# Optimization experiments

Measured on AMD Instinct MI355X. Metric: run time of the kernel, lower is better.

The kernel has to match this reference:

```python
import jax, jax.numpy as jnp
import numpy as np

C, K, DIL = 128, 3, 1
PAD = DIL
KK = K * K
EPS = 1e-5


def setup_inputs() -> dict:
    key = jax.random.key(0)
    k0, k1, k2 = jax.random.split(key, 3)
    B, H, W = 8, 128, 128
    x = jax.random.normal(k0, (B, C, H, W), jnp.float32)
    # small offset-conv weights so predicted offsets are realistic (sub-pixel scale)
    w_off = jax.random.normal(k1, (2 * KK, C, K, K), jnp.float32) * 0.01
    b_off = jnp.zeros((2 * KK,), jnp.float32)
    w_dw = jax.random.normal(k2, (C, 1, K, K), jnp.float32) * (1.0 / 3.0)
    gamma = jnp.ones((C,), jnp.float32)
    beta = jnp.zeros((C,), jnp.float32)
    return {"x": x, "w_off": w_off, "b_off": b_off, "w_dw": w_dw,
            "gamma": gamma, "beta": beta}


def _deform_depthwise(x, offset, w_dw):
    """torchvision-style deform_conv2d, groups=C (depthwise), stride=1."""
    B, C_, H, W = x.shape
    off = offset.reshape(B, KK, 2, H, W)  # (y,x) pairs per kernel tap
    hs = jnp.arange(H, dtype=x.dtype)[None, None, :, None]
    ws = jnp.arange(W, dtype=x.dtype)[None, None, None, :]
    ki = jnp.arange(K, dtype=x.dtype)
    ky = jnp.repeat(ki, K)  # [KK] row index of tap
    kx = jnp.tile(ki, K)    # [KK] col index of tap
    # sampling positions: base grid + dilated tap offset - pad + learned offset
    py = hs + (DIL * ky - PAD)[None, :, None, None] + off[:, :, 0]  # [B,KK,H,W]
    px = ws + (DIL * kx - PAD)[None, :, None, None] + off[:, :, 1]
    y0 = jnp.floor(py)
    x0 = jnp.floor(px)
    ty = py - y0
    tx = px - x0
    y0i = y0.astype(jnp.int32)
    x0i = x0.astype(jnp.int32)

    def gather(xb, yi, xi):
        # zero outside the image (torchvision zero-pad semantics)
        valid = (yi >= 0) & (yi < H) & (xi >= 0) & (xi < W)
        yc = jnp.clip(yi, 0, H - 1)
        xc = jnp.clip(xi, 0, W - 1)
        v = xb[:, yc, xc]  # [C,KK,H,W]
        return v * valid[None].astype(xb.dtype)

    def sample_one(xb, y0b, x0b, tyb, txb):
        v00 = gather(xb, y0b, x0b)
        v01 = gather(xb, y0b, x0b + 1)
        v10 = gather(xb, y0b + 1, x0b)
        v11 = gather(xb, y0b + 1, x0b + 1)
        w00 = (1 - tyb) * (1 - txb)
        w01 = (1 - tyb) * txb
        w10 = tyb * (1 - txb)
        w11 = tyb * txb
        return (v00 * w00[None] + v01 * w01[None]
                + v10 * w10[None] + v11 * w11[None])  # [C,KK,H,W]

    val = jax.vmap(sample_one)(x, y0i, x0i, ty, tx)  # [B,C,KK,H,W]
    # depthwise contraction over the KK taps
    return jnp.einsum('bckhw,ck->bchw', val, w_dw.reshape(C, KK))


def reference(x, w_off, b_off, w_dw, gamma, beta):
    identity = x
    offset = jax.lax.conv_general_dilated(
        x, w_off, window_strides=(1, 1), padding=[(PAD, PAD), (PAD, PAD)],
        dimension_numbers=('NCHW', 'OIHW', 'NCHW'))
    offset = offset + b_off[None, :, None, None]
    out = _deform_depthwise(x, offset, w_dw)
    # BatchNorm2d in training mode (batch statistics), then SiLU
    mean = jnp.mean(out, axis=(0, 2, 3), keepdims=True)
    var = jnp.mean((out - mean) ** 2, axis=(0, 2, 3), keepdims=True)
    out = (out - mean) * jax.lax.rsqrt(var + EPS)
    out = out * gamma[None, :, None, None] + beta[None, :, None, None]
    out = out * jax.nn.sigmoid(out)  # SiLU
    return out + identity
```

## Files before the change

kernel.cpp:

```cpp
#include <hip/hip_runtime.h>
#include <hip/hip_fp16.h>
#include <math.h>

#define Cc 128
#define Hh 128
#define Ww 128
#define Bb 8
#define HW 16384
#define NPIX 131072
#define NOFF 18

typedef unsigned int u32;
typedef __attribute__((ext_vector_type(8)))  short bf16x8;
typedef __attribute__((ext_vector_type(16))) float f32x16;

static __device__ __forceinline__ u32 f2bf(float f){
  u32 u = __float_as_uint(f);
  return (u + 0x7fffu + ((u >> 16) & 1u)) >> 16;
}

__global__ __launch_bounds__(256) void k_repack(const float* __restrict__ w_off, const float* __restrict__ w_dw,
                                                u32* __restrict__ wBf, float* __restrict__ wdt){
  int i = blockIdx.x*256 + threadIdx.x;
  if (i < 72*64*4){
    int step = i >> 8;
    int r    = i & 255;
    int lane = r >> 2;
    int q    = r & 3;
    int tap  = step / 8, chunk = step % 8;
    int o    = lane & 31, half = lane >> 5;
    int c0   = chunk*16 + half*8 + 2*q;
    float v0 = (o < NOFF) ? w_off[(size_t)(o*Cc + c0    )*9 + tap] : 0.f;
    float v1 = (o < NOFF) ? w_off[(size_t)(o*Cc + c0 + 1)*9 + tap] : 0.f;
    wBf[i] = f2bf(v0) | (f2bf(v1) << 16);
  }
  int j = i - 72*64*4;
  if (j >= 0 && j < 9*Cc){
    int c = j % Cc; int k = j / Cc;
    wdt[j] = w_dw[c*9 + k];
  }
}

__global__ __launch_bounds__(256) void k_tx(const float* __restrict__ x, u32* __restrict__ xt16){
  __shared__ float t[128][65];
  int tid = threadIdx.x;
  int b   = blockIdx.x >> 8;
  int hw0 = (blockIdx.x & 255) << 6;
  int lane = tid & 63, wg = tid >> 6;
  const float* xb = x + (size_t)b*Cc*HW;
  #pragma unroll
  for (int k=0;k<32;k++){
    int c = wg + k*4;
    t[c][lane] = xb[(size_t)c*HW + hw0 + lane];
  }
  __syncthreads();
  u32* ob = xt16 + ((size_t)b*HW + hw0)*64;
  int cpair = tid & 63, grp = tid >> 6;
  #pragma unroll
  for (int k=0;k<16;k++){
    int hwl = grp + k*4;
    float lo = t[cpair*2][hwl];
    float hi = t[cpair*2+1][hwl];
    ob[(size_t)hwl*64 + cpair] = f2bf(lo) | (f2bf(hi) << 16);
  }
}

__global__ __launch_bounds__(256) void k_offset_mfma(const u32* __restrict__ xt, const u32* __restrict__ wBf,
                                                     const float* __restrict__ b_off, u32* __restrict__ recs){
  __shared__ float piv[128][21];
  int tid = threadIdx.x, lane = tid & 63, wid = tid >> 6;
  int b = blockIdx.x >> 7, h = blockIdx.x & 127;
  int row = lane & 31, half = lane >> 5;
  int w0 = wid*32;
  int w = w0 + row;

  const u32* xb = xt + (size_t)b*HW*64;

  int taddr[9]; bool tval[9];
  #pragma unroll
  for (int t=0;t<9;t++){
    int ky = t/3 - 1, kx = t%3 - 1;
    int hh = h + ky, wt = w + kx;
    bool v = (hh>=0)&&(hh<Hh)&&(wt>=0)&&(wt<Ww);
    int hwd = hh*Ww + wt;
    hwd = min(max(hwd,0),HW-1);
    taddr[t] = hwd*64 + half*4;
    tval[t] = v;
  }

  f32x16 acc;
  #pragma unroll
  for (int i=0;i<16;i++) acc[i] = 0.f;

  const uint4* wb = (const uint4*)wBf;
  #pragma unroll 1
  for (int t=0;t<9;t++){
    const uint4* ap = (const uint4*)(xb + taddr[t]);
    bool v = tval[t];
    #pragma unroll
    for (int ch=0;ch<8;ch++){
      uint4 a = ap[ch*2];
      if (!v){ a.x=0u; a.y=0u; a.z=0u; a.w=0u; }
      uint4 bf = wb[(t*8+ch)*64 + lane];
      acc = __builtin_amdgcn_mfma_f32_32x32x16_bf16(*(bf16x8*)&a, *(bf16x8*)&bf, acc, 0, 0, 0);
    }
  }

  int o = lane & 31;
  #pragma unroll
  for (int r=0;r<16;r++){
    int pxl = w0 + ((r&3) + 8*(r>>2) + 4*half);
    if (o < NOFF) piv[pxl][o] = acc[r];
  }
  __syncthreads();

  if (tid < 128){
    int wpx = tid;
    float v[NOFF];
    #pragma unroll
    for (int oo=0;oo<NOFF;oo++) v[oo] = piv[wpx][oo] + b_off[oo];

    u32 rec[36];
    #pragma unroll
    for (int kk=0;kk<9;kk++){
      float py = (float)(h + kk/3 - 1) + v[2*kk];
      float qx = (float)(wpx + kk%3 - 1) + v[2*kk+1];
      float fy = floorf(py), fx = floorf(qx);
      float ty = py - fy, tx = qx - fx;
      int y0 = (int)fy, x0 = (int)fx;
      int y1 = y0+1, x1 = x0+1;
      bool vy0 = (y0>=0)&&(y0<Hh), vy1=(y1>=0)&&(y1<Hh);
      bool vx0 = (x0>=0)&&(x0<Ww), vx1=(x1>=0)&&(x1<Ww);
      u32 yc0 = (u32)(min(max(y0,0),Hh-1)*Ww), yc1 = (u32)(min(max(y1,0),Hh-1)*Ww);
      u32 xc0 = (u32)min(max(x0,0),Ww-1),      xc1 = (u32)min(max(x1,0),Ww-1);
      rec[2*kk]   = (yc0+xc0) | ((yc0+xc1)<<16);
      rec[2*kk+1] = (yc1+xc0) | ((yc1+xc1)<<16);
      float c00 = (vy0&&vx0) ? (1.f-ty)*(1.f-tx) : 0.f;
      float c01 = (vy0&&vx1) ? (1.f-ty)*tx       : 0.f;
      float c10 = (vy1&&vx0) ? ty*(1.f-tx)       : 0.f;
      float c11 = (vy1&&vx1) ? ty*tx             : 0.f;
      __half2 hA = __floats2half2_rn(c00, c01);
      __half2 hB = __floats2half2_rn(c10, c11);
      rec[18+2*kk] = *(u32*)&hA;
      rec[19+2*kk] = *(u32*)&hB;
    }
    int pxg = blockIdx.x*128 + wpx;
    uint4* dst = (uint4*)(recs + (size_t)pxg*36);
    #pragma unroll
    for (int q=0;q<9;q++) dst[q] = *(uint4*)(rec + q*4);
  }
}

__global__ __launch_bounds__(256) void k_deform_rec(const u32* __restrict__ xt, const u32* __restrict__ recs,
                                                    const float* __restrict__ wdt, float* __restrict__ out){
  __shared__ float pivot[16][132];
  int tid = threadIdx.x, lane = tid & 63, wid = tid >> 6;
  int pxb = blockIdx.x * 16;
  int bu = pxb >> 14, hw0 = pxb & 16383;
  int l2 = lane*2;

  float2 wk[9];
  #pragma unroll
  for (int k=0;k<9;k++) wk[k] = *(const float2*)(wdt + k*Cc + l2);

  const u32* xbu = xt + (size_t)bu*HW*64;

  #pragma unroll
  for (int i=0;i<4;i++){
    int pu = __builtin_amdgcn_readfirstlane(pxb + wid*4 + i);
    const u32* rec = recs + (size_t)pu*36;

    u32 q[9][4];
    #pragma unroll
    for (int kk=0;kk<9;kk++){
      u32 dA = rec[2*kk], dB = rec[2*kk+1];
      q[kk][0] = xbu[(size_t)(dA & 0xFFFFu)*64 + lane];
      q[kk][1] = xbu[(size_t)(dA >> 16)   *64 + lane];
      q[kk][2] = xbu[(size_t)(dB & 0xFFFFu)*64 + lane];
      q[kk][3] = xbu[(size_t)(dB >> 16)   *64 + lane];
    }

    float acc0 = 0.f, acc1 = 0.f;
    #pragma unroll
    for (int kk=0;kk<9;kk++){
      u32 uA = rec[18+2*kk], uB = rec[19+2*kk];
      __half2 hA = *(__half2*)&uA, hB = *(__half2*)&uB;
      float c00 = __low2float(hA), c01 = __high2float(hA);
      float c10 = __low2float(hB), c11 = __high2float(hB);
      float v0l = __uint_as_float(q[kk][0] << 16), v0h = __uint_as_float(q[kk][0] & 0xffff0000u);
      float v1l = __uint_as_float(q[kk][1] << 16), v1h = __uint_as_float(q[kk][1] & 0xffff0000u);
      float v2l = __uint_as_float(q[kk][2] << 16), v2h = __uint_as_float(q[kk][2] & 0xffff0000u);
      float v3l = __uint_as_float(q[kk][3] << 16), v3h = __uint_as_float(q[kk][3] & 0xffff0000u);
      float s0 = c00*v0l; s0 = fmaf(c01, v1l, s0); s0 = fmaf(c10, v2l, s0); s0 = fmaf(c11, v3l, s0);
      float s1 = c00*v0h; s1 = fmaf(c01, v1h, s1); s1 = fmaf(c10, v2h, s1); s1 = fmaf(c11, v3h, s1);
      acc0 = fmaf(wk[kk].x, s0, acc0);
      acc1 = fmaf(wk[kk].y, s1, acc1);
    }
    pivot[wid*4+i][l2]   = acc0;
    pivot[wid*4+i][l2+1] = acc1;
  }
  __syncthreads();
  #pragma unroll
  for (int it=0; it<2; it++){
    int c = (tid>>2) + it*64, qd = tid & 3;
    float4 r = make_float4(pivot[qd*4+0][c], pivot[qd*4+1][c], pivot[qd*4+2][c], pivot[qd*4+3][c]);
    *(float4*)(out + ((size_t)bu*Cc + c)*HW + hw0 + qd*4) = r;
  }
}

__global__ __launch_bounds__(256) void k_stats1(const float* __restrict__ dw, float* __restrict__ ps){
  int c = blockIdx.x >> 3, b = blockIdx.x & 7;
  const float4* p = (const float4*)(dw + ((size_t)b*Cc + c)*HW);
  float s = 0.f, s2 = 0.f;
  for (int i=threadIdx.x; i<HW/4; i+=256){
    float4 v = p[i];
    s += v.x + v.y + v.z + v.w;
    s2 = fmaf(v.x, v.x, s2); s2 = fmaf(v.y, v.y, s2);
    s2 = fmaf(v.z, v.z, s2); s2 = fmaf(v.w, v.w, s2);
  }
  #pragma unroll
  for (int d=32; d>0; d>>=1){ s += __shfl_down(s, d, 64); s2 += __shfl_down(s2, d, 64); }
  __shared__ float ls[4], ls2[4];
  int lane = threadIdx.x & 63, wid = threadIdx.x >> 6;
  if (lane==0){ ls[wid]=s; ls2[wid]=s2; }
  __syncthreads();
  if (threadIdx.x==0){
    float S=0.f, S2=0.f;
    #pragma unroll
    for (int i=0;i<4;i++){ S+=ls[i]; S2+=ls2[i]; }
    ps[c*8+b] = S;
    ps[1024 + c*8+b] = S2;
  }
}

__global__ __launch_bounds__(128) void k_stats2(const float* __restrict__ ps, float* __restrict__ mr){
  int c = threadIdx.x;
  float S=0.f, S2=0.f;
  #pragma unroll
  for (int b=0;b<8;b++){ S += ps[c*8+b]; S2 += ps[1024 + c*8+b]; }
  const float invN = 1.f/(float)(Bb*HW);
  float m = S*invN;
  float var = S2*invN - m*m;
  mr[c]      = m;
  mr[Cc + c] = rsqrtf(var + 1e-5f);
}

__global__ __launch_bounds__(256) void k_apply(float* __restrict__ out, const float* __restrict__ x,
                                               const float* __restrict__ mr, const float* __restrict__ gamma,
                                               const float* __restrict__ beta){
  int i = blockIdx.x*256 + threadIdx.x;
  int c = (i >> 12) & 127;
  float4 v  = ((const float4*)out)[i];
  float4 xi = ((const float4*)x)[i];
  float m = mr[c], r = mr[Cc+c], g = gamma[c], be = beta[c];
  float* vp = (float*)&v; const float* xp = (const float*)&xi;
  float4 o; float* op = (float*)&o;
  #pragma unroll
  for (int j=0;j<4;j++){
    float t = (vp[j]-m)*r*g + be;
    t = t / (1.f + expf(-t));
    op[j] = t + xp[j];
  }
  ((float4*)out)[i] = o;
}

extern "C" void kernel_launch(void* const* d_in, const int* in_sizes, int n_in,
                              void* d_out, int out_size, void* d_ws, size_t ws_size,
                              hipStream_t stream) {
  const float* x     = (const float*)d_in[0];
  const float* w_off = (const float*)d_in[1];
  const float* b_off = (const float*)d_in[2];
  const float* w_dw  = (const float*)d_in[3];
  const float* gamma = (const float*)d_in[4];
  const float* beta  = (const float*)d_in[5];
  float* out = (float*)d_out;

  u32*   wBf = (u32*)d_ws;
  float* wdt = (float*)d_ws + 23040;
  float* mr  = (float*)d_ws + 24576;
  float* ps  = mr + 256;
  u32* recs  = (u32*)d_ws + 32768;
  u32* xt16  = recs + (size_t)NPIX*36;

  hipLaunchKernelGGL(k_repack, dim3((72*64*4 + 9*Cc + 255)/256), dim3(256), 0, stream, w_off, w_dw, wBf, wdt);
  hipLaunchKernelGGL(k_tx,     dim3(2048), dim3(256), 0, stream, x, xt16);
  hipLaunchKernelGGL(k_offset_mfma, dim3(1024), dim3(256), 0, stream, xt16, wBf, b_off, recs);
  hipLaunchKernelGGL(k_deform_rec,  dim3(NPIX/16), dim3(256), 0, stream, xt16, recs, wdt, out);
  hipLaunchKernelGGL(k_stats1, dim3(Cc*Bb), dim3(256), 0, stream, out, ps);
  hipLaunchKernelGGL(k_stats2, dim3(1),     dim3(128), 0, stream, ps, mr);
  hipLaunchKernelGGL(k_apply,  dim3(NPIX*Cc/4/256), dim3(256), 0, stream, out, x, mr, gamma, beta);
}
```

Baseline: 178.3 us.

## Fuse BN statistics into deform kernel and store intermediate as bf16

The deformable depthwise kernel now computes per-block partial sums and sums of squares for each channel. This replaces the separate stats pass, which re-read the whole fp32 intermediate. When the workspace is large enough, the intermediate is also written as bf16 to a workspace buffer, halving its write and read traffic, and the apply kernel decodes it. The cost is a two-stage reduction over 8192 block partials, plus reduced precision of the pre-BN activations, which could affect accuracy.

```diff
diff --git a/kernel.cpp b/kernel.cpp
--- a/kernel.cpp
+++ b/kernel.cpp
@@ -151,8 +151,10 @@
   }
 }
 
+template<bool BF16OUT>
 __global__ __launch_bounds__(256) void k_deform_rec(const u32* __restrict__ xt, const u32* __restrict__ recs,
-                                                    const float* __restrict__ wdt, float* __restrict__ out){
+                                                    const float* __restrict__ wdt, float* __restrict__ out,
+                                                    u32* __restrict__ dwb, float* __restrict__ bps){
   __shared__ float pivot[16][132];
   int tid = threadIdx.x, lane = tid & 63, wid = tid >> 6;
   int pxb = blockIdx.x * 16;
@@ -204,50 +206,53 @@
   for (int it=0; it<2; it++){
     int c = (tid>>2) + it*64, qd = tid & 3;
     float4 r = make_float4(pivot[qd*4+0][c], pivot[qd*4+1][c], pivot[qd*4+2][c], pivot[qd*4+3][c]);
-    *(float4*)(out + ((size_t)bu*Cc + c)*HW + hw0 + qd*4) = r;
-  }
-}
-
-__global__ __launch_bounds__(256) void k_stats1(const float* __restrict__ dw, float* __restrict__ ps){
-  int c = blockIdx.x >> 3, b = blockIdx.x & 7;
-  const float4* p = (const float4*)(dw + ((size_t)b*Cc + c)*HW);
-  float s = 0.f, s2 = 0.f;
-  for (int i=threadIdx.x; i<HW/4; i+=256){
-    float4 v = p[i];
-    s += v.x + v.y + v.z + v.w;
-    s2 = fmaf(v.x, v.x, s2); s2 = fmaf(v.y, v.y, s2);
-    s2 = fmaf(v.z, v.z, s2); s2 = fmaf(v.w, v.w, s2);
-  }
-  #pragma unroll
-  for (int d=32; d>0; d>>=1){ s += __shfl_down(s, d, 64); s2 += __shfl_down(s2, d, 64); }
-  __shared__ float ls[4], ls2[4];
-  int lane = threadIdx.x & 63, wid = threadIdx.x >> 6;
-  if (lane==0){ ls[wid]=s; ls2[wid]=s2; }
+    float s  = (r.x + r.y) + (r.z + r.w);
+    float s2 = fmaf(r.x,r.x, fmaf(r.y,r.y, fmaf(r.z,r.z, r.w*r.w)));
+    s  += __shfl_down(s, 2, 4);  s  += __shfl_down(s, 1, 4);
+    s2 += __shfl_down(s2, 2, 4); s2 += __shfl_down(s2, 1, 4);
+    if (qd == 0){
+      bps[(size_t)blockIdx.x*256 + c]       = s;
+      bps[(size_t)blockIdx.x*256 + 128 + c] = s2;
+    }
+    if (BF16OUT){
+      u32 p0 = f2bf(r.x) | (f2bf(r.y) << 16);
+      u32 p1 = f2bf(r.z) | (f2bf(r.w) << 16);
+      uint2 pp; pp.x = p0; pp.y = p1;
+      *(uint2*)&dwb[(((size_t)bu*Cc + c)*HW + hw0)/2 + qd*2] = pp;
+    } else {
+      *(float4*)(out + ((size_t)bu*Cc + c)*HW + hw0 + qd*4) = r;
+    }
+  }
+}
+
+__global__ __launch_bounds__(256) void k_statsr1(const float* __restrict__ bps, float* __restrict__ part2){
+  int tid = threadIdx.x;
+  size_t base = (size_t)blockIdx.x * 64;
+  float a = 0.f;
+  for (int r=0;r<64;r++) a += bps[(base + r)*256 + tid];
+  part2[blockIdx.x*256 + tid] = a;
+}
+
+__global__ __launch_bounds__(256) void k_statsr2(const float* __restrict__ part2, float* __restrict__ mr){
+  __shared__ float t[256];
+  int tid = threadIdx.x;
+  float a = 0.f;
+  for (int r=0;r<128;r++) a += part2[r*256 + tid];
+  t[tid] = a;
   __syncthreads();
-  if (threadIdx.x==0){
-    float S=0.f, S2=0.f;
-    #pragma unroll
-    for (int i=0;i<4;i++){ S+=ls[i]; S2+=ls2[i]; }
-    ps[c*8+b] = S;
-    ps[1024 + c*8+b] = S2;
-  }
-}
-
-__global__ __launch_bounds__(128) void k_stats2(const float* __restrict__ ps, float* __restrict__ mr){
-  int c = threadIdx.x;
-  float S=0.f, S2=0.f;
-  #pragma unroll
-  for (int b=0;b<8;b++){ S += ps[c*8+b]; S2 += ps[1024 + c*8+b]; }
-  const float invN = 1.f/(float)(Bb*HW);
-  float m = S*invN;
-  float var = S2*invN - m*m;
-  mr[c]      = m;
-  mr[Cc + c] = rsqrtf(var + 1e-5f);
-}
-
-__global__ __launch_bounds__(256) void k_apply(float* __restrict__ out, const float* __restrict__ x,
-                                               const float* __restrict__ mr, const float* __restrict__ gamma,
-                                               const float* __restrict__ beta){
+  if (tid < 128){
+    float S = t[tid], S2 = t[128 + tid];
+    const float invN = 1.f/(float)(Bb*HW);
+    float m = S*invN;
+    float var = S2*invN - m*m;
+    mr[tid]       = m;
+    mr[Cc + tid]  = rsqrtf(var + 1e-5f);
+  }
+}
+
+__global__ __launch_bounds__(256) void k_apply_f32(float* __restrict__ out, const float* __restrict__ x,
+                                                   const float* __restrict__ mr, const float* __restrict__ gamma,
+                                                   const float* __restrict__ beta){
   int i = blockIdx.x*256 + threadIdx.x;
   int c = (i >> 12) & 127;
   float4 v  = ((const float4*)out)[i];
@@ -258,6 +263,30 @@
   #pragma unroll
   for (int j=0;j<4;j++){
     float t = (vp[j]-m)*r*g + be;
+    t = t / (1.f + expf(-t));
+    op[j] = t + xp[j];
+  }
+  ((float4*)out)[i] = o;
+}
+
+__global__ __launch_bounds__(256) void k_apply_bf16(const u32* __restrict__ dwb, float* __restrict__ out,
+                                                    const float* __restrict__ x, const float* __restrict__ mr,
+                                                    const float* __restrict__ gamma, const float* __restrict__ beta){
+  int i = blockIdx.x*256 + threadIdx.x;
+  int c = (i >> 12) & 127;
+  uint2 dw = ((const uint2*)dwb)[i];
+  float4 xi = ((const float4*)x)[i];
+  float m = mr[c], r = mr[Cc+c], g = gamma[c], be = beta[c];
+  float v[4];
+  v[0] = __uint_as_float(dw.x << 16);
+  v[1] = __uint_as_float(dw.x & 0xffff0000u);
+  v[2] = __uint_as_float(dw.y << 16);
+  v[3] = __uint_as_float(dw.y & 0xffff0000u);
+  const float* xp = (const float*)&xi;
+  float4 o; float* op = (float*)&o;
+  #pragma unroll
+  for (int j=0;j<4;j++){
+    float t = (v[j]-m)*r*g + be;
     t = t / (1.f + expf(-t));
     op[j] = t + xp[j];
   }
@@ -275,18 +304,33 @@
   const float* beta  = (const float*)d_in[5];
   float* out = (float*)d_out;
 
-  u32*   wBf = (u32*)d_ws;
-  float* wdt = (float*)d_ws + 23040;
-  float* mr  = (float*)d_ws + 24576;
-  float* ps  = mr + 256;
-  u32* recs  = (u32*)d_ws + 32768;
-  u32* xt16  = recs + (size_t)NPIX*36;
+  u32*   wBf  = (u32*)d_ws;
+  float* wdt  = (float*)d_ws + 23040;
+  float* mr   = (float*)d_ws + 24576;
+  u32*   recs = (u32*)d_ws + 32768;
+  u32*   xt16 = recs + (size_t)NPIX*36;
+  float* bps  = (float*)(xt16 + (size_t)NPIX*64);
+  float* part2= bps + (size_t)8192*256;
+  u32*   dwb  = (u32*)(part2 + 128*256);
+
+  const size_t NEED_B = ((size_t)32768 + (size_t)NPIX*36 + (size_t)NPIX*64
+                         + (size_t)8192*256 + 128*256 + (size_t)NPIX*64) * 4;
+  bool big = (ws_size >= NEED_B);
 
   hipLaunchKernelGGL(k_repack, dim3((72*64*4 + 9*Cc + 255)/256), dim3(256), 0, stream, w_off, w_dw, wBf, wdt);
   hipLaunchKernelGGL(k_tx,     dim3(2048), dim3(256), 0, stream, x, xt16);
   hipLaunchKernelGGL(k_offset_mfma, dim3(1024), dim3(256), 0, stream, xt16, wBf, b_off, recs);
-  hipLaunchKernelGGL(k_deform_rec,  dim3(NPIX/16), dim3(256), 0, stream, xt16, recs, wdt, out);
-  hipLaunchKernelGGL(k_stats1, dim3(Cc*Bb), dim3(256), 0, stream, out, ps);
-  hipLaunchKernelGGL(k_stats2, dim3(1),     dim3(128), 0, stream, ps, mr);
-  hipLaunchKernelGGL(k_apply,  dim3(NPIX*Cc/4/256), dim3(256), 0, stream, out, x, mr, gamma, beta);
-}
+
+  if (big){
+    hipLaunchKernelGGL((k_deform_rec<true>), dim3(NPIX/16), dim3(256), 0, stream, xt16, recs, wdt, out, dwb, bps);
+  } else {
+    hipLaunchKernelGGL((k_deform_rec<false>), dim3(NPIX/16), dim3(256), 0, stream, xt16, recs, wdt, out, dwb, bps);
+  }
+  hipLaunchKernelGGL(k_statsr1, dim3(128), dim3(256), 0, stream, bps, part2);
+  hipLaunchKernelGGL(k_statsr2, dim3(1),   dim3(256), 0, stream, part2, mr);
+  if (big){
+    hipLaunchKernelGGL(k_apply_bf16, dim3(NPIX*Cc/4/256), dim3(256), 0, stream, dwb, out, x, mr, gamma, beta);
+  } else {
+    hipLaunchKernelGGL(k_apply_f32,  dim3(NPIX*Cc/4/256), dim3(256), 0, stream, out, x, mr, gamma, beta);
+  }
+}
```

Result: faster. 171.1 us (-4.0%).
